# Optimization experiments

Measured on AMD Instinct MI355X. Metric: run time of the kernel, lower is better.

Reference implementation:

```python
import jax, jax.numpy as jnp
import numpy as np

DIM = 512
HEADS = 8
ALPHA = 0.5
HIDDEN = int(DIM * 2.0)
EPS = 1e-5


def _layernorm(x, g, b):
    mu = jnp.mean(x, axis=-1, keepdims=True)
    var = jnp.var(x, axis=-1, keepdims=True)
    return (x - mu) * jax.lax.rsqrt(var + EPS) * g + b


def setup_inputs() -> dict:
    key = jax.random.key(0)
    ks = jax.random.split(key, 8)
    B, N, C = 4, 1536, DIM
    s = lambda fan_in: 1.0 / np.sqrt(fan_in)
    return {
        "x": jax.random.normal(ks[0], (B, N, C), dtype=jnp.float32),
        "ln1_g": jnp.ones((C,), jnp.float32),
        "ln1_b": jnp.zeros((C,), jnp.float32),
        "qkv_w": jax.random.normal(ks[1], (C, 3 * C), jnp.float32) * s(C),
        "qkv_b": jnp.zeros((3 * C,), jnp.float32),
        "ln2_g": jnp.ones((C,), jnp.float32),
        "ln2_b": jnp.zeros((C,), jnp.float32),
        "fc1_w": jax.random.normal(ks[2], (C, HIDDEN), jnp.float32) * s(C),
        "fc1_b": jnp.zeros((HIDDEN,), jnp.float32),
        "fc2_w": jax.random.normal(ks[3], (HIDDEN, C), jnp.float32) * s(HIDDEN),
        "fc2_b": jnp.zeros((C,), jnp.float32),
    }


def reference(x, ln1_g, ln1_b, qkv_w, qkv_b, ln2_g, ln2_b, fc1_w, fc1_b, fc2_w, fc2_b):
    B, N, C = x.shape
    H = HEADS
    d = C // H
    S = N // 3

    h = _layernorm(x, ln1_g, ln1_b)
    qkv = (h @ qkv_w + qkv_b).reshape(B, N, 3, H, d)
    qkv = jnp.transpose(qkv, (2, 0, 3, 1, 4))  # [3,B,H,N,d]
    q, k, v = qkv[0], qkv[1], qkv[2]

    attn = jnp.einsum('bhnd,bhmd->bhnm', q, k) * (d ** -0.5)  # [B,H,N,N]
    # sequential cross-segment score mixing (matches in-place torch semantics)
    s0 = attn[:, :, 0:S]
    s1 = attn[:, :, S:2 * S] + ALPHA * s0
    s2 = attn[:, :, 2 * S:] + ALPHA * s1
    attn = jnp.concatenate([s0, s1, s2], axis=2)
    attn = jax.nn.softmax(attn, axis=-1)

    o = jnp.einsum('bhnm,bhmd->bhnd', attn, v)
    o = jnp.transpose(o, (0, 2, 1, 3)).reshape(B, N, C)
    x = x + o  # NOTE: self.proj is defined but unused in the original forward

    h2 = _layernorm(x, ln2_g, ln2_b)
    m = jax.nn.gelu(h2 @ fc1_w + fc1_b, approximate=False) @ fc2_w + fc2_b
    return x + m
```

## Files before the change

### kernel.cpp

```cpp
#include <hip/hip_runtime.h>
#include <hip/hip_bf16.h>
#include <math.h>

#define DIMC 512
#define NSEQ 1536
#define BATCH 4
#define NHEADS 8
#define HDIM 64
#define SSEG 512
#define HIDDEN_DIM 1024
#define ALPHA_C 0.5f
#define EPS_C 1e-5f
#define NROWS (BATCH*NSEQ)
#define SHIFT_C 6.0f

typedef __attribute__((ext_vector_type(8))) short bfrag8;
typedef __attribute__((ext_vector_type(8))) _Float16 hfrag8;
typedef __attribute__((ext_vector_type(4))) float ffrag;
typedef float4 f4;

__device__ __forceinline__ ushort f2bf(float v) {
    __hip_bfloat16 hb = __float2bfloat16(v);
    return *(ushort*)&hb;
}

__device__ __forceinline__ void gl2lds16(const ushort* g, ushort* l) {
    __builtin_amdgcn_global_load_lds(
        (const __attribute__((address_space(1))) unsigned*)g,
        (__attribute__((address_space(3))) unsigned*)l, 16, 0, 0);
}

__global__ __launch_bounds__(256)
void prep_kernel(const float* __restrict__ qkv_w, const float* __restrict__ fc1_w,
                 const float* __restrict__ fc2_w, ushort* __restrict__ qkv_wt,
                 ushort* __restrict__ fc1_wt, ushort* __restrict__ fc2_wt,
                 const float* __restrict__ x, const float* __restrict__ g,
                 const float* __restrict__ bvec, ushort* __restrict__ h_out)
{
    int bid = blockIdx.x;
    if (bid < 448) {
        __shared__ float tile[64][65];
        const float* W; ushort* Wt; int K, N, n0, k0;
        if (bid < 192)      { W = qkv_w; Wt = qkv_wt; K = 512;  N = 1536; int b = bid;       n0 = (b % 24) * 64; k0 = (b / 24) * 64; }
        else if (bid < 320) { W = fc1_w; Wt = fc1_wt; K = 512;  N = 1024; int b = bid - 192; n0 = (b % 16) * 64; k0 = (b / 16) * 64; }
        else                { W = fc2_w; Wt = fc2_wt; K = 1024; N = 512;  int b = bid - 320; n0 = (b % 8)  * 64; k0 = (b / 8)  * 64; }
        int tx = threadIdx.x & 63, ty = threadIdx.x >> 6;
        #pragma unroll
        for (int i = 0; i < 16; i++) {
            int r = i * 4 + ty;
            tile[r][tx] = W[(size_t)(k0 + r) * N + n0 + tx];
        }
        __syncthreads();
        #pragma unroll
        for (int i = 0; i < 16; i++) {
            int r = i * 4 + ty;
            Wt[(size_t)(n0 + r) * K + k0 + tx] = f2bf(tile[tx][r]);
        }
    } else {
        __shared__ float red[16];
        int row = bid - 448;
        int t = threadIdx.x;
        int lane = t & 63, w = t >> 6;
        const float* rp = x + (size_t)row * DIMC;
        float v0 = rp[t];
        float v1 = rp[t + 256];
        float s = v0 + v1;
        float s2 = v0 * v0 + v1 * v1;
        #pragma unroll
        for (int o = 32; o > 0; o >>= 1) {
            s  += __shfl_down(s,  o, 64);
            s2 += __shfl_down(s2, o, 64);
        }
        if (lane == 0) { red[w] = s; red[8 + w] = s2; }
        __syncthreads();
        if (t == 0) {
            float a = red[0] + red[1] + red[2] + red[3];
            float c = red[8] + red[9] + red[10] + red[11];
            red[0] = a; red[8] = c;
        }
        __syncthreads();
        float mean = red[0] * (1.0f / DIMC);
        float var  = red[8] * (1.0f / DIMC) - mean * mean;
        float rstd = rsqrtf(var + EPS_C);
        ushort* op = h_out + (size_t)row * DIMC;
        op[t]       = f2bf((v0 - mean) * rstd * g[t]       + bvec[t]);
        op[t + 256] = f2bf((v1 - mean) * rstd * g[t + 256] + bvec[t + 256]);
    }
}

__global__ __launch_bounds__(256)
void ln_kernel(const float* __restrict__ in, const float* __restrict__ g,
               const float* __restrict__ b, ushort* __restrict__ out)
{
    __shared__ float red[16];
    int row = blockIdx.x;
    int t = threadIdx.x;
    int lane = t & 63, w = t >> 6;
    const float* rp = in + (size_t)row * DIMC;
    float v0 = rp[t];
    float v1 = rp[t + 256];
    float s = v0 + v1;
    float s2 = v0 * v0 + v1 * v1;
    #pragma unroll
    for (int o = 32; o > 0; o >>= 1) {
        s  += __shfl_down(s,  o, 64);
        s2 += __shfl_down(s2, o, 64);
    }
    if (lane == 0) { red[w] = s; red[8 + w] = s2; }
    __syncthreads();
    if (t == 0) {
        float a = red[0] + red[1] + red[2] + red[3];
        float c = red[8] + red[9] + red[10] + red[11];
        red[0] = a; red[8] = c;
    }
    __syncthreads();
    float mean = red[0] * (1.0f / DIMC);
    float var  = red[8] * (1.0f / DIMC) - mean * mean;
    float rstd = rsqrtf(var + EPS_C);
    ushort* op = out + (size_t)row * DIMC;
    op[t]       = f2bf((v0 - mean) * rstd * g[t]       + b[t]);
    op[t + 256] = f2bf((v1 - mean) * rstd * g[t + 256] + b[t + 256]);
}

template <int EPI>
__global__ __launch_bounds__(256)
void mgemm_kernel(const ushort* __restrict__ A, const ushort* __restrict__ Wt,
                  const float* __restrict__ bias, const float* resid,
                  void* out, int M, int K, int Nn)
{
    __shared__ ushort As[2][2][64 * 32];
    __shared__ ushort Bs[2][2][64 * 32];
    int tid = threadIdx.x;
    int lane = tid & 63, w = tid >> 6;
    int cl = lane & 15, qg = lane >> 4;
    int wm = w >> 1, wn = w & 1;
    int rowBase = blockIdx.y * 64, colBase = blockIdx.x * 64;
    int sr = lane >> 2;
    int sb = (lane & 3) * 8;

    const ushort* agb = A  + (size_t)(rowBase + w * 16 + sr) * K + sb;
    const ushort* bgb = Wt + (size_t)(colBase + w * 16 + sr) * K + sb;

    ffrag acc[2][2];
    #pragma unroll
    for (int mi = 0; mi < 2; mi++)
        #pragma unroll
        for (int ni = 0; ni < 2; ni++)
            #pragma unroll
            for (int r = 0; r < 4; r++) acc[mi][ni][r] = 0.f;

    int niter = K >> 6;

    #pragma unroll
    for (int hf = 0; hf < 2; hf++) {
        gl2lds16(agb + hf * 32, &As[0][hf][(w * 16) * 32]);
        gl2lds16(bgb + hf * 32, &Bs[0][hf][(w * 16) * 32]);
    }
    __syncthreads();

    for (int it = 0; it < niter; it++) {
        int cur = it & 1;
        if (it + 1 < niter) {
            int k0 = (it + 1) * 64;
            #pragma unroll
            for (int hf = 0; hf < 2; hf++) {
                gl2lds16(agb + k0 + hf * 32, &As[cur ^ 1][hf][(w * 16) * 32]);
                gl2lds16(bgb + k0 + hf * 32, &Bs[cur ^ 1][hf][(w * 16) * 32]);
            }
        }
        #pragma unroll
        for (int ks = 0; ks < 2; ks++) {
            bfrag8 af[2], bf[2];
            #pragma unroll
            for (int mi = 0; mi < 2; mi++)
                af[mi] = *(const bfrag8*)&As[cur][ks][(wm * 32 + mi * 16 + cl) * 32 + qg * 8];
            #pragma unroll
            for (int ni = 0; ni < 2; ni++)
                bf[ni] = *(const bfrag8*)&Bs[cur][ks][(wn * 32 + ni * 16 + cl) * 32 + qg * 8];
            #pragma unroll
            for (int mi = 0; mi < 2; mi++)
                #pragma unroll
                for (int ni = 0; ni < 2; ni++)
                    acc[mi][ni] = __builtin_amdgcn_mfma_f32_16x16x32_bf16(af[mi], bf[ni], acc[mi][ni], 0, 0, 0);
        }
        if (it + 1 < niter) __syncthreads();
    }

    #pragma unroll
    for (int mi = 0; mi < 2; mi++) {
        #pragma unroll
        for (int ni = 0; ni < 2; ni++) {
            #pragma unroll
            for (int r = 0; r < 4; r++) {
                int row = rowBase + wm * 32 + mi * 16 + qg * 4 + r;
                int col = colBase + wn * 32 + ni * 16 + cl;
                float v = acc[mi][ni][r] + (EPI == 3 ? bias[row] : bias[col]);
                if (EPI == 1) v = 0.5f * v * (1.0f + erff(v * 0.70710678118654752f));
                if (EPI == 2) {
                    v += resid[(size_t)row * Nn + col];
                    ((float*)out)[(size_t)row * Nn + col] = v;
                } else if (EPI == 3) {
                    _Float16 e = (_Float16)v;
                    int t = col & 31;
                    int pcol = (col & ~31) | (((t & 15) >> 2) * 8 + (t >> 4) * 4 + (t & 3));
                    ((ushort*)out)[(size_t)row * Nn + pcol] = *(ushort*)&e;
                } else {
                    ((ushort*)out)[(size_t)row * Nn + col] = f2bf(v);
                }
            }
        }
    }
}

__global__ __launch_bounds__(256)
void attn_kernel(const ushort* __restrict__ qk, const ushort* __restrict__ vt,
                 const float* __restrict__ x, float* __restrict__ xres)
{
    __shared__ float Op[48][68];
    __shared__ float Lp[4][4][16][3];

    int qi0 = blockIdx.x * 16;
    int bh  = blockIdx.y;
    int b = bh >> 3, h = bh & 7;
    int tid = threadIdx.x;
    int lane = tid & 63, w = tid >> 6;
    int cl = lane & 15, qg = lane >> 4;

    const ushort* base = qk + (size_t)b * NSEQ * 1024 + h * HDIM;
    const _Float16* vbase = (const _Float16*)vt + (size_t)(h * HDIM) * NROWS + b * NSEQ;
    const float scale = 0.125f;

    bfrag8 bq[3][2];
    #pragma unroll
    for (int seg = 0; seg < 3; seg++)
        #pragma unroll
        for (int f = 0; f < 2; f++)
            bq[seg][f] = *(const bfrag8*)(base + (size_t)(seg * SSEG + qi0 + cl) * 1024 + f * 32 + qg * 8);

    ffrag o[3][4];
    #pragma unroll
    for (int seg = 0; seg < 3; seg++)
        #pragma unroll
        for (int mg = 0; mg < 4; mg++)
            #pragma unroll
            for (int r = 0; r < 4; r++) o[seg][mg][r] = 0.f;
    float lp[3] = {0.f, 0.f, 0.f};

    int kb = w * 384;

    #pragma unroll 1
    for (int it = 0; it < 12; it++) {
        int k0 = kb + it * 32;

        hfrag8 av[4];
        #pragma unroll
        for (int mg = 0; mg < 4; mg++)
            av[mg] = *(const hfrag8*)(vbase + (size_t)(mg * 16 + cl) * NROWS + k0 + qg * 8);

        bfrag8 af[2][2];
        #pragma unroll
        for (int s = 0; s < 2; s++)
            #pragma unroll
            for (int f = 0; f < 2; f++)
                af[s][f] = *(const bfrag8*)(base + (size_t)(k0 + s * 16 + cl) * 1024 + 512 + f * 32 + qg * 8);

        float p[2][3][4];
        #pragma unroll
        for (int s = 0; s < 2; s++) {
            #pragma unroll
            for (int seg = 0; seg < 3; seg++) {
                ffrag c;
                #pragma unroll
                for (int r = 0; r < 4; r++) c[r] = 0.f;
                c = __builtin_amdgcn_mfma_f32_16x16x32_bf16(af[s][0], bq[seg][0], c, 0, 0, 0);
                c = __builtin_amdgcn_mfma_f32_16x16x32_bf16(af[s][1], bq[seg][1], c, 0, 0, 0);
                #pragma unroll
                for (int r = 0; r < 4; r++) p[s][seg][r] = c[r];
            }
        }

        #pragma unroll
        for (int s = 0; s < 2; s++) {
            #pragma unroll
            for (int r = 0; r < 4; r++) {
                float s0 = p[s][0][r] * scale;
                float s1 = p[s][1][r] * scale + ALPHA_C * s0;
                float s2 = p[s][2][r] * scale + ALPHA_C * s1;
                float e0 = __expf(s0 - SHIFT_C);
                float e1 = __expf(s1 - SHIFT_C);
                float e2 = __expf(s2 - SHIFT_C);
                p[s][0][r] = e0; p[s][1][r] = e1; p[s][2][r] = e2;
                lp[0] += e0; lp[1] += e1; lp[2] += e2;
            }
        }

        hfrag8 bp[3];
        #pragma unroll
        for (int seg = 0; seg < 3; seg++)
            #pragma unroll
            for (int j = 0; j < 4; j++) {
                bp[seg][j]     = (_Float16)p[0][seg][j];
                bp[seg][4 + j] = (_Float16)p[1][seg][j];
            }

        #pragma unroll
        for (int mg = 0; mg < 4; mg++)
            #pragma unroll
            for (int seg = 0; seg < 3; seg++)
                o[seg][mg] = __builtin_amdgcn_mfma_f32_16x16x32_f16(av[mg], bp[seg], o[seg][mg], 0, 0, 0);
    }

    #pragma unroll
    for (int seg = 0; seg < 3; seg++) Lp[w][qg][cl][seg] = lp[seg];

    #pragma unroll 1
    for (int wv = 0; wv < 4; wv++) {
        __syncthreads();
        if (w == wv) {
            #pragma unroll
            for (int seg = 0; seg < 3; seg++)
                #pragma unroll
                for (int mg = 0; mg < 4; mg++) {
                    float* dst = &Op[seg * 16 + cl][mg * 16 + qg * 4];
                    if (wv == 0) {
                        #pragma unroll
                        for (int r = 0; r < 4; r++) dst[r] = o[seg][mg][r];
                    } else {
                        #pragma unroll
                        for (int r = 0; r < 4; r++) dst[r] += o[seg][mg][r];
                    }
                }
        }
    }
    __syncthreads();

    if (tid < 192) {
        int row = tid >> 2;
        int seg = row >> 4, q16 = row & 15;
        int d0 = (tid & 3) * 16;
        float l = 0.f;
        #pragma unroll
        for (int wv = 0; wv < 4; wv++)
            #pragma unroll
            for (int g2 = 0; g2 < 4; g2++)
                l += Lp[wv][g2][q16][seg];
        float invl = 1.0f / l;
        size_t rowg = ((size_t)(b * NSEQ + seg * SSEG + qi0 + q16)) * DIMC + h * HDIM + d0;
        #pragma unroll
        for (int dd = 0; dd < 16; dd += 4) {
            f4 xv = *(const f4*)(x + rowg + dd);
            f4 ov;
            ov.x = Op[row][d0 + dd + 0] * invl + xv.x;
            ov.y = Op[row][d0 + dd + 1] * invl + xv.y;
            ov.z = Op[row][d0 + dd + 2] * invl + xv.z;
            ov.w = Op[row][d0 + dd + 3] * invl + xv.w;
            *(f4*)(xres + rowg + dd) = ov;
        }
    }
}

extern "C" void kernel_launch(void* const* d_in, const int* in_sizes, int n_in,
                              void* d_out, int out_size, void* d_ws, size_t ws_size,
                              hipStream_t stream)
{
    const float* x     = (const float*)d_in[0];
    const float* ln1_g = (const float*)d_in[1];
    const float* ln1_b = (const float*)d_in[2];
    const float* qkv_w = (const float*)d_in[3];
    const float* qkv_b = (const float*)d_in[4];
    const float* ln2_g = (const float*)d_in[5];
    const float* ln2_b = (const float*)d_in[6];
    const float* fc1_w = (const float*)d_in[7];
    const float* fc1_b = (const float*)d_in[8];
    const float* fc2_w = (const float*)d_in[9];
    const float* fc2_b = (const float*)d_in[10];
    float* out = (float*)d_out;

    char* p = (char*)d_ws;
    ushort* h_bf    = (ushort*)p;  p += (size_t)NROWS * DIMC * 2;
    ushort* qkb     = (ushort*)p;  p += (size_t)NROWS * 2 * DIMC * 2;
    ushort* vtb     = (ushort*)p;  p += (size_t)DIMC * NROWS * 2;
    ushort* mid     = (ushort*)p;  p += (size_t)NROWS * HIDDEN_DIM * 2;
    ushort* qkv_wt  = (ushort*)p;  p += (size_t)3 * DIMC * DIMC * 2;
    ushort* fc1_wt  = (ushort*)p;  p += (size_t)HIDDEN_DIM * DIMC * 2;
    ushort* fc2_wt  = (ushort*)p;
    float* xres = out;

    prep_kernel<<<448 + NROWS, 256, 0, stream>>>(qkv_w, fc1_w, fc2_w, qkv_wt, fc1_wt, fc2_wt,
                                                 x, ln1_g, ln1_b, h_bf);

    mgemm_kernel<0><<<dim3(2 * DIMC / 64, NROWS / 64), 256, 0, stream>>>(
        h_bf, qkv_wt, qkv_b, nullptr, (void*)qkb, NROWS, DIMC, 2 * DIMC);

    mgemm_kernel<3><<<dim3(NROWS / 64, DIMC / 64), 256, 0, stream>>>(
        qkv_wt + (size_t)2 * DIMC * DIMC, h_bf, qkv_b + 2 * DIMC, nullptr,
        (void*)vtb, DIMC, DIMC, NROWS);

    attn_kernel<<<dim3(SSEG / 16, BATCH * NHEADS), 256, 0, stream>>>(qkb, vtb, x, xres);

    ln_kernel<<<NROWS, 256, 0, stream>>>(xres, ln2_g, ln2_b, h_bf);

    mgemm_kernel<1><<<dim3(HIDDEN_DIM / 64, NROWS / 64), 256, 0, stream>>>(
        h_bf, fc1_wt, fc1_b, nullptr, (void*)mid, NROWS, DIMC, HIDDEN_DIM);

    mgemm_kernel<2><<<dim3(DIMC / 64, NROWS / 64), 256, 0, stream>>>(
        mid, fc2_wt, fc2_b, xres, (void*)out, NROWS, HIDDEN_DIM, DIMC);
}
```

Baseline: 219.8 us.

## Merge QK and V-transpose GEMMs, remap attention blocks, double-buffer attention loads

```diff
diff --git a/kernel.cpp b/kernel.cpp
--- a/kernel.cpp
+++ b/kernel.cpp
@@ -123,18 +123,17 @@
 }
 
 template <int EPI>
-__global__ __launch_bounds__(256)
-void mgemm_kernel(const ushort* __restrict__ A, const ushort* __restrict__ Wt,
-                  const float* __restrict__ bias, const float* resid,
-                  void* out, int M, int K, int Nn)
-{
-    __shared__ ushort As[2][2][64 * 32];
-    __shared__ ushort Bs[2][2][64 * 32];
+__device__ __forceinline__
+void mgemm_body(const ushort* __restrict__ A, const ushort* __restrict__ Wt,
+                const float* __restrict__ bias, const float* resid,
+                void* out, int M, int K, int Nn, int bx, int by,
+                ushort* As, ushort* Bs)
+{
     int tid = threadIdx.x;
     int lane = tid & 63, w = tid >> 6;
     int cl = lane & 15, qg = lane >> 4;
     int wm = w >> 1, wn = w & 1;
-    int rowBase = blockIdx.y * 64, colBase = blockIdx.x * 64;
+    int rowBase = by * 64, colBase = bx * 64;
     int sr = lane >> 2;
     int sb = (lane & 3) * 8;
 
@@ -153,8 +152,8 @@
 
     #pragma unroll
     for (int hf = 0; hf < 2; hf++) {
-        gl2lds16(agb + hf * 32, &As[0][hf][(w * 16) * 32]);
-        gl2lds16(bgb + hf * 32, &Bs[0][hf][(w * 16) * 32]);
+        gl2lds16(agb + hf * 32, As + (0 * 2 + hf) * 2048 + (w * 16) * 32);
+        gl2lds16(bgb + hf * 32, Bs + (0 * 2 + hf) * 2048 + (w * 16) * 32);
     }
     __syncthreads();
 
@@ -164,8 +163,8 @@
             int k0 = (it + 1) * 64;
             #pragma unroll
             for (int hf = 0; hf < 2; hf++) {
-                gl2lds16(agb + k0 + hf * 32, &As[cur ^ 1][hf][(w * 16) * 32]);
-                gl2lds16(bgb + k0 + hf * 32, &Bs[cur ^ 1][hf][(w * 16) * 32]);
+                gl2lds16(agb + k0 + hf * 32, As + ((cur ^ 1) * 2 + hf) * 2048 + (w * 16) * 32);
+                gl2lds16(bgb + k0 + hf * 32, Bs + ((cur ^ 1) * 2 + hf) * 2048 + (w * 16) * 32);
             }
         }
         #pragma unroll
@@ -173,10 +172,10 @@
             bfrag8 af[2], bf[2];
             #pragma unroll
             for (int mi = 0; mi < 2; mi++)
-                af[mi] = *(const bfrag8*)&As[cur][ks][(wm * 32 + mi * 16 + cl) * 32 + qg * 8];
+                af[mi] = *(const bfrag8*)&As[(cur * 2 + ks) * 2048 + (wm * 32 + mi * 16 + cl) * 32 + qg * 8];
             #pragma unroll
             for (int ni = 0; ni < 2; ni++)
-                bf[ni] = *(const bfrag8*)&Bs[cur][ks][(wn * 32 + ni * 16 + cl) * 32 + qg * 8];
+                bf[ni] = *(const bfrag8*)&Bs[(cur * 2 + ks) * 2048 + (wn * 32 + ni * 16 + cl) * 32 + qg * 8];
             #pragma unroll
             for (int mi = 0; mi < 2; mi++)
                 #pragma unroll
@@ -212,6 +211,35 @@
     }
 }
 
+template <int EPI>
+__global__ __launch_bounds__(256)
+void mgemm_kernel(const ushort* __restrict__ A, const ushort* __restrict__ Wt,
+                  const float* __restrict__ bias, const float* resid,
+                  void* out, int M, int K, int Nn)
+{
+    __shared__ ushort As[2 * 2 * 64 * 32];
+    __shared__ ushort Bs[2 * 2 * 64 * 32];
+    mgemm_body<EPI>(A, Wt, bias, resid, out, M, K, Nn, blockIdx.x, blockIdx.y, As, Bs);
+}
+
+__global__ __launch_bounds__(256)
+void qkvt_kernel(const ushort* __restrict__ h_bf, const ushort* __restrict__ qkv_wt,
+                 const float* __restrict__ qkv_b, ushort* __restrict__ qkb,
+                 ushort* __restrict__ vtb)
+{
+    __shared__ ushort As[2 * 2 * 64 * 32];
+    __shared__ ushort Bs[2 * 2 * 64 * 32];
+    int bid = blockIdx.x;
+    if (bid < 1536) {
+        mgemm_body<0>(h_bf, qkv_wt, qkv_b, nullptr, (void*)qkb,
+                      NROWS, DIMC, 2 * DIMC, bid & 15, bid >> 4, As, Bs);
+    } else {
+        int b2 = bid - 1536;
+        mgemm_body<3>(qkv_wt + (size_t)2 * DIMC * DIMC, h_bf, qkv_b + 2 * DIMC, nullptr,
+                      (void*)vtb, DIMC, DIMC, NROWS, b2 % 96, b2 / 96, As, Bs);
+    }
+}
+
 __global__ __launch_bounds__(256)
 void attn_kernel(const ushort* __restrict__ qk, const ushort* __restrict__ vt,
                  const float* __restrict__ x, float* __restrict__ xres)
@@ -219,8 +247,10 @@
     __shared__ float Op[48][68];
     __shared__ float Lp[4][4][16][3];
 
-    int qi0 = blockIdx.x * 16;
-    int bh  = blockIdx.y;
+    int n = blockIdx.x + (blockIdx.y << 5);
+    int idx = n >> 3;
+    int bh  = (n & 7) * 4 + (idx & 3);
+    int qi0 = (idx >> 2) * 16;
     int b = bh >> 3, h = bh & 7;
     int tid = threadIdx.x;
     int lane = tid & 63, w = tid >> 6;
@@ -248,22 +278,18 @@
 
     int kb = w * 384;
 
-    #pragma unroll 1
-    for (int it = 0; it < 12; it++) {
-        int k0 = kb + it * 32;
-
-        hfrag8 av[4];
+    auto loadf = [&](int k0, hfrag8* av, bfrag8 (*af)[2]) {
         #pragma unroll
         for (int mg = 0; mg < 4; mg++)
             av[mg] = *(const hfrag8*)(vbase + (size_t)(mg * 16 + cl) * NROWS + k0 + qg * 8);
-
-        bfrag8 af[2][2];
         #pragma unroll
         for (int s = 0; s < 2; s++)
             #pragma unroll
             for (int f = 0; f < 2; f++)
                 af[s][f] = *(const bfrag8*)(base + (size_t)(k0 + s * 16 + cl) * 1024 + 512 + f * 32 + qg * 8);
-
+    };
+
+    auto comp = [&](const hfrag8* av, const bfrag8 (*af)[2]) {
         float p[2][3][4];
         #pragma unroll
         for (int s = 0; s < 2; s++) {
@@ -278,7 +304,6 @@
                 for (int r = 0; r < 4; r++) p[s][seg][r] = c[r];
             }
         }
-
         #pragma unroll
         for (int s = 0; s < 2; s++) {
             #pragma unroll
@@ -293,7 +318,6 @@
                 lp[0] += e0; lp[1] += e1; lp[2] += e2;
             }
         }
-
         hfrag8 bp[3];
         #pragma unroll
         for (int seg = 0; seg < 3; seg++)
@@ -302,12 +326,22 @@
                 bp[seg][j]     = (_Float16)p[0][seg][j];
                 bp[seg][4 + j] = (_Float16)p[1][seg][j];
             }
-
         #pragma unroll
         for (int mg = 0; mg < 4; mg++)
             #pragma unroll
             for (int seg = 0; seg < 3; seg++)
                 o[seg][mg] = __builtin_amdgcn_mfma_f32_16x16x32_f16(av[mg], bp[seg], o[seg][mg], 0, 0, 0);
+    };
+
+    hfrag8 avA[4], avB[4];
+    bfrag8 afA[2][2], afB[2][2];
+    loadf(kb, avA, afA);
+    #pragma unroll 1
+    for (int it = 0; it < 12; it += 2) {
+        loadf(kb + (it + 1) * 32, avB, afB);
+        comp(avA, afA);
+        if (it + 2 < 12) loadf(kb + (it + 2) * 32, avA, afA);
+        comp(avB, afB);
     }
 
     #pragma unroll
@@ -389,12 +423,7 @@
     prep_kernel<<<448 + NROWS, 256, 0, stream>>>(qkv_w, fc1_w, fc2_w, qkv_wt, fc1_wt, fc2_wt,
                                                  x, ln1_g, ln1_b, h_bf);
 
-    mgemm_kernel<0><<<dim3(2 * DIMC / 64, NROWS / 64), 256, 0, stream>>>(
-        h_bf, qkv_wt, qkv_b, nullptr, (void*)qkb, NROWS, DIMC, 2 * DIMC);
-
-    mgemm_kernel<3><<<dim3(NROWS / 64, DIMC / 64), 256, 0, stream>>>(
-        qkv_wt + (size_t)2 * DIMC * DIMC, h_bf, qkv_b + 2 * DIMC, nullptr,
-        (void*)vtb, DIMC, DIMC, NROWS);
+    qkvt_kernel<<<2304, 256, 0, stream>>>(h_bf, qkv_wt, qkv_b, qkb, vtb);
 
     attn_kernel<<<dim3(SSEG / 16, BATCH * NHEADS), 256, 0, stream>>>(qkb, vtb, x, xres);
 
```

Result: no change. 216.7 us (-1.4%).
